# Optimization experiments

Hardware: AMD Instinct MI355X
Metric: run time of the kernel (lower is better)

The kernel has to match this reference:

```python
import jax, jax.numpy as jnp
import numpy as np

N_NODES = 25000
IN_DIM = 16
EDGE_DIM = 8
HID = 32
OUT_DIM = 16
N_EDGES = 400000
MLP_HID = 32


def setup_inputs() -> dict:
    key = jax.random.key(0)
    ks = jax.random.split(key, 12)
    x = jax.random.normal(ks[0], (N_NODES, IN_DIM), dtype=jnp.float32)
    edge_index = jax.random.randint(ks[1], (2, N_EDGES), 0, N_NODES, dtype=jnp.int32)
    edge_attr = jax.random.normal(ks[2], (N_EDGES, EDGE_DIM), dtype=jnp.float32)
    s = lambda fan_in: 1.0 / np.sqrt(fan_in)
    W1 = jax.random.uniform(ks[3], (EDGE_DIM, MLP_HID), minval=-s(EDGE_DIM), maxval=s(EDGE_DIM))
    b1 = jax.random.uniform(ks[4], (MLP_HID,), minval=-s(EDGE_DIM), maxval=s(EDGE_DIM))
    W2 = jax.random.uniform(ks[5], (MLP_HID, IN_DIM * HID), minval=-s(MLP_HID), maxval=s(MLP_HID))
    b2 = jax.random.uniform(ks[6], (IN_DIM * HID,), minval=-s(MLP_HID), maxval=s(MLP_HID))
    root = jax.random.uniform(ks[7], (IN_DIM, HID), minval=-s(IN_DIM), maxval=s(IN_DIM))
    bias = jnp.zeros((HID,), dtype=jnp.float32)
    Wlin = jax.random.uniform(ks[8], (HID, OUT_DIM), minval=-s(HID), maxval=s(HID))
    blin = jax.random.uniform(ks[9], (OUT_DIM,), minval=-s(HID), maxval=s(HID))
    return {"x": x, "edge_attr": edge_attr, "W1": W1, "b1": b1, "W2": W2,
            "b2": b2, "root": root, "bias": bias, "Wlin": Wlin, "blin": blin,
            "edge_index": edge_index}


def reference(x, edge_attr, W1, b1, W2, b2, root, bias, Wlin, blin, edge_index):
    src, dst = edge_index[0], edge_index[1]  # x_j gathered from src, aggregated at dst
    # edge MLP -> per-edge weight matrix [E, IN_DIM, HID]
    h = jax.nn.relu(edge_attr @ W1 + b1)
    W_e = (h @ W2 + b2).reshape(-1, IN_DIM, HID)
    # gather source features and per-edge matvec: [E, HID]
    msg = jnp.einsum('ei,eio->eo', x[src], W_e)
    # scatter-mean over target nodes
    agg = jax.ops.segment_sum(msg, dst, num_segments=N_NODES)
    cnt = jax.ops.segment_sum(jnp.ones((msg.shape[0],), dtype=msg.dtype), dst, num_segments=N_NODES)
    agg = agg / jnp.maximum(cnt, 1.0)[:, None]
    # NNConv root weight + bias, then ReLU and final linear
    out = jax.nn.relu(agg + x @ root + bias)
    return out @ Wlin + blin
```

## Files before the change

kernel.cpp:

```cpp
#include <hip/hip_runtime.h>
#include <cstdint>

#define E_EDGES 400000
#define N_NODES 25000
#define GROUPS  (E_EDGES/16)
#define NPACK   18432

typedef float f32x4 __attribute__((ext_vector_type(4)));
typedef __bf16 bf16x8 __attribute__((ext_vector_type(8)));

static __device__ __forceinline__ ushort f2bf(float f) {
    union { __bf16 b; ushort u; } c; c.b = (__bf16)f; return c.u;
}

__global__ void __launch_bounds__(256) k_pack(const float* __restrict__ W2,
                                              const float* __restrict__ b2,
                                              const float* __restrict__ W1,
                                              ushort* __restrict__ packed) {
    int t = blockIdx.x * 256 + threadIdx.x;
    if (t >= NPACK) return;
    float v = 0.0f;
    if (t < 17408) {
        int j  = t & 7;
        int ln = (t >> 3) & 15;
        int kg = (t >> 7) & 3;
        int nt = (t >> 9) & 1;
        int kt = t >> 10;
        int kap = (j < 4) ? (kg * 4 + j) : (16 + kg * 4 + (j - 4));
        if (kt < 16)       v = W2[kap * 512 + kt * 32 + nt * 16 + ln];
        else if (kap < 16) v = b2[kap * 32 + nt * 16 + ln];
    } else {
        int idx  = t - 17408;
        int half = idx >> 9;
        int lane = (idx >> 3) & 63;
        int j    = idx & 7;
        int kg = lane >> 4, ln = lane & 15;
        if (kg == 0) v = W1[j * 32 + half * 16 + ln];
    }
    packed[t] = f2bf(v);
}

__global__ void __launch_bounds__(256, 4) k_edge(const float* __restrict__ ea,
                                                 const float* __restrict__ x,
                                                 const int* __restrict__ ei,
                                                 const ushort* __restrict__ packed,
                                                 const float* __restrict__ b1,
                                                 float* __restrict__ agg,
                                                 uint* __restrict__ cnt_u) {
    __shared__ alignas(16) ushort w2l[NPACK];
    __shared__ float b1l[32];
    {
        const uint4* s = (const uint4*)packed;
        uint4* d = (uint4*)w2l;
        for (int i = threadIdx.x; i < NPACK / 8; i += 256) d[i] = s[i];
        if (threadIdx.x < 32) b1l[threadIdx.x] = b1[threadIdx.x];
    }
    __syncthreads();

    const int lane = threadIdx.x & 63;
    const int ln = lane & 15;
    const int kg = lane >> 4;
    const int gp = blockIdx.x * 4 + (threadIdx.x >> 6);
    const int g0 = gp * 2, g1 = g0 + 1;
    const int e0 = g0 * 16 + ln, e1 = g1 * 16 + ln;

    const int s0  = ei[e0],            s1  = ei[e1];
    const int dc0 = ei[E_EDGES + e0],  dc1 = ei[E_EDGES + e1];
    const int r0 = g0 * 16 + kg * 4, r1 = g1 * 16 + kg * 4;
    const int d00 = ei[E_EDGES + r0 + 0], d01 = ei[E_EDGES + r0 + 1];
    const int d02 = ei[E_EDGES + r0 + 2], d03 = ei[E_EDGES + r0 + 3];
    const int d10 = ei[E_EDGES + r1 + 0], d11 = ei[E_EDGES + r1 + 1];
    const int d12 = ei[E_EDGES + r1 + 2], d13 = ei[E_EDGES + r1 + 3];

    const f32x4* xp0 = (const f32x4*)(x + (size_t)s0 * 16);
    const f32x4 xa0 = xp0[0], xa1 = xp0[1], xa2 = xp0[2], xa3 = xp0[3];
    const f32x4* xp1 = (const f32x4*)(x + (size_t)s1 * 16);
    const f32x4 xb0 = xp1[0], xb1 = xp1[1], xb2 = xp1[2], xb3 = xp1[3];

    const f32x4* ep0 = (const f32x4*)(ea + (size_t)e0 * 8);
    const f32x4 ea00 = ep0[0], ea01 = ep0[1];
    const f32x4* ep1 = (const f32x4*)(ea + (size_t)e1 * 8);
    const f32x4 ea10 = ep1[0], ea11 = ep1[1];

    bf16x8 eb0, eb1;
    if (kg == 0) {
        eb0[0]=(__bf16)ea00[0]; eb0[1]=(__bf16)ea00[1]; eb0[2]=(__bf16)ea00[2]; eb0[3]=(__bf16)ea00[3];
        eb0[4]=(__bf16)ea01[0]; eb0[5]=(__bf16)ea01[1]; eb0[6]=(__bf16)ea01[2]; eb0[7]=(__bf16)ea01[3];
        eb1[0]=(__bf16)ea10[0]; eb1[1]=(__bf16)ea10[1]; eb1[2]=(__bf16)ea10[2]; eb1[3]=(__bf16)ea10[3];
        eb1[4]=(__bf16)ea11[0]; eb1[5]=(__bf16)ea11[1]; eb1[6]=(__bf16)ea11[2]; eb1[7]=(__bf16)ea11[3];
    } else {
        const __bf16 z = (__bf16)0.0f;
        eb0[0]=z; eb0[1]=z; eb0[2]=z; eb0[3]=z; eb0[4]=z; eb0[5]=z; eb0[6]=z; eb0[7]=z;
        eb1 = eb0;
    }

    const bf16x8 aw0 = *(const bf16x8*)(&w2l[17408 + lane * 8]);
    const bf16x8 aw1 = *(const bf16x8*)(&w2l[17408 + 512 + lane * 8]);
    f32x4 z4 = {0.f, 0.f, 0.f, 0.f};
    f32x4 hA0 = __builtin_amdgcn_mfma_f32_16x16x32_bf16(aw0, eb0, z4, 0, 0, 0);
    f32x4 hA1 = __builtin_amdgcn_mfma_f32_16x16x32_bf16(aw1, eb0, z4, 0, 0, 0);
    f32x4 hB0 = __builtin_amdgcn_mfma_f32_16x16x32_bf16(aw0, eb1, z4, 0, 0, 0);
    f32x4 hB1 = __builtin_amdgcn_mfma_f32_16x16x32_bf16(aw1, eb1, z4, 0, 0, 0);

    float h0[8], h1[8];
#pragma unroll
    for (int r = 0; r < 4; ++r) {
        const float blo = b1l[4 * kg + r], bhi = b1l[16 + 4 * kg + r];
        h0[r]     = fmaxf(hA0[r] + blo, 0.f);
        h0[4 + r] = fmaxf(hA1[r] + bhi, 0.f);
        h1[r]     = fmaxf(hB0[r] + blo, 0.f);
        h1[4 + r] = fmaxf(hB1[r] + bhi, 0.f);
    }

    float xr0[16], xr1[16];
    xr0[0]=xa0[0]; xr0[1]=xa0[1]; xr0[2]=xa0[2]; xr0[3]=xa0[3];
    xr0[4]=xa1[0]; xr0[5]=xa1[1]; xr0[6]=xa1[2]; xr0[7]=xa1[3];
    xr0[8]=xa2[0]; xr0[9]=xa2[1]; xr0[10]=xa2[2]; xr0[11]=xa2[3];
    xr0[12]=xa3[0]; xr0[13]=xa3[1]; xr0[14]=xa3[2]; xr0[15]=xa3[3];
    xr1[0]=xb0[0]; xr1[1]=xb0[1]; xr1[2]=xb0[2]; xr1[3]=xb0[3];
    xr1[4]=xb1[0]; xr1[5]=xb1[1]; xr1[6]=xb1[2]; xr1[7]=xb1[3];
    xr1[8]=xb2[0]; xr1[9]=xb2[1]; xr1[10]=xb2[2]; xr1[11]=xb2[3];
    xr1[12]=xb3[0]; xr1[13]=xb3[1]; xr1[14]=xb3[2]; xr1[15]=xb3[3];

    f32x4 acc00 = z4, acc01 = z4, acc10 = z4, acc11 = z4;

#pragma unroll
    for (int kt = 0; kt < 16; ++kt) {
        const bf16x8 bf0 = *(const bf16x8*)(&w2l[(kt * 2 + 0) * 512 + lane * 8]);
        const bf16x8 bf1 = *(const bf16x8*)(&w2l[(kt * 2 + 1) * 512 + lane * 8]);
        const float xv0 = xr0[kt], xv1 = xr1[kt];
        bf16x8 a0, a1;
#pragma unroll
        for (int j = 0; j < 8; ++j) {
            a0[j] = (__bf16)(xv0 * h0[j]);
            a1[j] = (__bf16)(xv1 * h1[j]);
        }
        acc00 = __builtin_amdgcn_mfma_f32_16x16x32_bf16(a0, bf0, acc00, 0, 0, 0);
        acc10 = __builtin_amdgcn_mfma_f32_16x16x32_bf16(a1, bf0, acc10, 0, 0, 0);
        acc01 = __builtin_amdgcn_mfma_f32_16x16x32_bf16(a0, bf1, acc01, 0, 0, 0);
        acc11 = __builtin_amdgcn_mfma_f32_16x16x32_bf16(a1, bf1, acc11, 0, 0, 0);
    }
    {
        const f32x4 xs0 = (kg == 0) ? xa0 : ((kg == 1) ? xa1 : ((kg == 2) ? xa2 : xa3));
        const f32x4 xs1 = (kg == 0) ? xb0 : ((kg == 1) ? xb1 : ((kg == 2) ? xb2 : xb3));
        const __bf16 z = (__bf16)0.0f;
        bf16x8 a0, a1;
        a0[0]=(__bf16)xs0[0]; a0[1]=(__bf16)xs0[1]; a0[2]=(__bf16)xs0[2]; a0[3]=(__bf16)xs0[3];
        a0[4]=z; a0[5]=z; a0[6]=z; a0[7]=z;
        a1[0]=(__bf16)xs1[0]; a1[1]=(__bf16)xs1[1]; a1[2]=(__bf16)xs1[2]; a1[3]=(__bf16)xs1[3];
        a1[4]=z; a1[5]=z; a1[6]=z; a1[7]=z;
        const bf16x8 bf0 = *(const bf16x8*)(&w2l[(16 * 2 + 0) * 512 + lane * 8]);
        const bf16x8 bf1 = *(const bf16x8*)(&w2l[(16 * 2 + 1) * 512 + lane * 8]);
        acc00 = __builtin_amdgcn_mfma_f32_16x16x32_bf16(a0, bf0, acc00, 0, 0, 0);
        acc10 = __builtin_amdgcn_mfma_f32_16x16x32_bf16(a1, bf0, acc10, 0, 0, 0);
        acc01 = __builtin_amdgcn_mfma_f32_16x16x32_bf16(a0, bf1, acc01, 0, 0, 0);
        acc11 = __builtin_amdgcn_mfma_f32_16x16x32_bf16(a1, bf1, acc11, 0, 0, 0);
    }

    atomicAdd(&agg[d00 * 32 + ln], acc00[0]);
    atomicAdd(&agg[d01 * 32 + ln], acc00[1]);
    atomicAdd(&agg[d02 * 32 + ln], acc00[2]);
    atomicAdd(&agg[d03 * 32 + ln], acc00[3]);
    atomicAdd(&agg[d00 * 32 + 16 + ln], acc01[0]);
    atomicAdd(&agg[d01 * 32 + 16 + ln], acc01[1]);
    atomicAdd(&agg[d02 * 32 + 16 + ln], acc01[2]);
    atomicAdd(&agg[d03 * 32 + 16 + ln], acc01[3]);
    atomicAdd(&agg[d10 * 32 + ln], acc10[0]);
    atomicAdd(&agg[d11 * 32 + ln], acc10[1]);
    atomicAdd(&agg[d12 * 32 + ln], acc10[2]);
    atomicAdd(&agg[d13 * 32 + ln], acc10[3]);
    atomicAdd(&agg[d10 * 32 + 16 + ln], acc11[0]);
    atomicAdd(&agg[d11 * 32 + 16 + ln], acc11[1]);
    atomicAdd(&agg[d12 * 32 + 16 + ln], acc11[2]);
    atomicAdd(&agg[d13 * 32 + 16 + ln], acc11[3]);

    if (kg == 0) {
        atomicAdd(&cnt_u[dc0], 1u);
        atomicAdd(&cnt_u[dc1], 1u);
    }
}

__global__ void __launch_bounds__(256) k_node(const float* __restrict__ agg,
                                              const uint* __restrict__ cnt_u,
                                              const float* __restrict__ x,
                                              const float* __restrict__ root,
                                              const float* __restrict__ bias,
                                              const float* __restrict__ Wlin,
                                              const float* __restrict__ blin,
                                              float* __restrict__ out) {
    __shared__ float al[256];
    const int n0 = blockIdx.x * 8;
    const int t = threadIdx.x;
    const int n = n0 + (t >> 5), h = t & 31;
    float a = 0.0f;
    if (n < N_NODES) {
        const float c = (float)cnt_u[n];
        float s = agg[n * 32 + h] / fmaxf(c, 1.0f) + bias[h];
        const f32x4* xp = (const f32x4*)(x + (size_t)n * 16);
        const f32x4 x0 = xp[0], x1 = xp[1], x2 = xp[2], x3 = xp[3];
        float xv[16];
        xv[0]=x0[0]; xv[1]=x0[1]; xv[2]=x0[2]; xv[3]=x0[3];
        xv[4]=x1[0]; xv[5]=x1[1]; xv[6]=x1[2]; xv[7]=x1[3];
        xv[8]=x2[0]; xv[9]=x2[1]; xv[10]=x2[2]; xv[11]=x2[3];
        xv[12]=x3[0]; xv[13]=x3[1]; xv[14]=x3[2]; xv[15]=x3[3];
#pragma unroll
        for (int i = 0; i < 16; ++i) s += xv[i] * root[i * 32 + h];
        a = fmaxf(s, 0.0f);
    }
    al[t] = a;
    __syncthreads();
    if (t < 128) {
        const int nj = n0 + (t >> 4), j = t & 15;
        if (nj < N_NODES) {
            float s = blin[j];
#pragma unroll
            for (int h2 = 0; h2 < 32; ++h2) s += al[(t >> 4) * 32 + h2] * Wlin[h2 * 16 + j];
            out[nj * 16 + j] = s;
        }
    }
}

extern "C" void kernel_launch(void* const* d_in, const int* in_sizes, int n_in,
                              void* d_out, int out_size, void* d_ws, size_t ws_size,
                              hipStream_t stream) {
    const float* x    = (const float*)d_in[0];
    const float* ea   = (const float*)d_in[1];
    const float* W1   = (const float*)d_in[2];
    const float* b1   = (const float*)d_in[3];
    const float* W2   = (const float*)d_in[4];
    const float* b2   = (const float*)d_in[5];
    const float* root = (const float*)d_in[6];
    const float* bias = (const float*)d_in[7];
    const float* Wlin = (const float*)d_in[8];
    const float* blin = (const float*)d_in[9];
    const int*   ei   = (const int*)d_in[10];
    float* out = (float*)d_out;

    char* ws = (char*)d_ws;
    float*  agg    = (float*)(ws + 0);
    uint*   cnt_u  = (uint*)(ws + 3200000);
    ushort* packed = (ushort*)(ws + 3300000);

    hipMemsetAsync(d_ws, 0, 3300000, stream);

    k_pack<<<(NPACK + 255) / 256, 256, 0, stream>>>(W2, b2, W1, packed);
    k_edge<<<3125, 256, 0, stream>>>(ea, x, ei, packed, b1, agg, cnt_u);
    k_node<<<3125, 256, 0, stream>>>(agg, cnt_u, x, root, bias, Wlin, blin, out);
}
```

Measured before the change: 86.08 us.

## Halve edge-kernel grid with two-unit persistent loop, prefetch, and move counts to pack kernel

The edge kernel now launches about half as many blocks. Each wave processes up to two 32-edge units and prefetches the next unit's indices and edge attributes while computing the current one. This amortizes the per-block LDS weight load, which is about 36 KB. Destination indices are loaded as int4 vectors, and in-degree counting moves into the pack kernel, which now covers all edges. The risks are higher register pressure from the prefetch, the dropped occupancy launch bound, and less parallelism in the edge kernel.

```diff
diff --git a/kernel.cpp b/kernel.cpp
--- a/kernel.cpp
+++ b/kernel.cpp
@@ -3,8 +3,10 @@
 
 #define E_EDGES 400000
 #define N_NODES 25000
-#define GROUPS  (E_EDGES/16)
+#define NU      12500
 #define NPACK   18432
+#define BLOCKS  1563
+#define NWAVES  (BLOCKS*4)
 
 typedef float f32x4 __attribute__((ext_vector_type(4)));
 typedef __bf16 bf16x8 __attribute__((ext_vector_type(8)));
@@ -16,37 +18,40 @@
 __global__ void __launch_bounds__(256) k_pack(const float* __restrict__ W2,
                                               const float* __restrict__ b2,
                                               const float* __restrict__ W1,
-                                              ushort* __restrict__ packed) {
+                                              const int* __restrict__ ei,
+                                              ushort* __restrict__ packed,
+                                              uint* __restrict__ cnt_u) {
     int t = blockIdx.x * 256 + threadIdx.x;
-    if (t >= NPACK) return;
-    float v = 0.0f;
-    if (t < 17408) {
-        int j  = t & 7;
-        int ln = (t >> 3) & 15;
-        int kg = (t >> 7) & 3;
-        int nt = (t >> 9) & 1;
-        int kt = t >> 10;
-        int kap = (j < 4) ? (kg * 4 + j) : (16 + kg * 4 + (j - 4));
-        if (kt < 16)       v = W2[kap * 512 + kt * 32 + nt * 16 + ln];
-        else if (kap < 16) v = b2[kap * 32 + nt * 16 + ln];
-    } else {
-        int idx  = t - 17408;
-        int half = idx >> 9;
-        int lane = (idx >> 3) & 63;
-        int j    = idx & 7;
-        int kg = lane >> 4, ln = lane & 15;
-        if (kg == 0) v = W1[j * 32 + half * 16 + ln];
-    }
-    packed[t] = f2bf(v);
-}
-
-__global__ void __launch_bounds__(256, 4) k_edge(const float* __restrict__ ea,
-                                                 const float* __restrict__ x,
-                                                 const int* __restrict__ ei,
-                                                 const ushort* __restrict__ packed,
-                                                 const float* __restrict__ b1,
-                                                 float* __restrict__ agg,
-                                                 uint* __restrict__ cnt_u) {
+    if (t < NPACK) {
+        float v = 0.0f;
+        if (t < 17408) {
+            int j  = t & 7;
+            int ln = (t >> 3) & 15;
+            int kg = (t >> 7) & 3;
+            int nt = (t >> 9) & 1;
+            int kt = t >> 10;
+            int kap = (j < 4) ? (kg * 4 + j) : (16 + kg * 4 + (j - 4));
+            if (kt < 16)       v = W2[kap * 512 + kt * 32 + nt * 16 + ln];
+            else if (kap < 16) v = b2[kap * 32 + nt * 16 + ln];
+        } else {
+            int idx  = t - 17408;
+            int half = idx >> 9;
+            int lane = (idx >> 3) & 63;
+            int j    = idx & 7;
+            int kg = lane >> 4, ln = lane & 15;
+            if (kg == 0) v = W1[j * 32 + half * 16 + ln];
+        }
+        packed[t] = f2bf(v);
+    }
+    if (t < E_EDGES) atomicAdd(&cnt_u[ei[E_EDGES + t]], 1u);
+}
+
+__global__ void __launch_bounds__(256) k_edge(const float* __restrict__ ea,
+                                              const float* __restrict__ x,
+                                              const int* __restrict__ ei,
+                                              const ushort* __restrict__ packed,
+                                              const float* __restrict__ b1,
+                                              float* __restrict__ agg) {
     __shared__ alignas(16) ushort w2l[NPACK];
     __shared__ float b1l[32];
     {
@@ -60,123 +65,137 @@
     const int lane = threadIdx.x & 63;
     const int ln = lane & 15;
     const int kg = lane >> 4;
-    const int gp = blockIdx.x * 4 + (threadIdx.x >> 6);
-    const int g0 = gp * 2, g1 = g0 + 1;
-    const int e0 = g0 * 16 + ln, e1 = g1 * 16 + ln;
-
-    const int s0  = ei[e0],            s1  = ei[e1];
-    const int dc0 = ei[E_EDGES + e0],  dc1 = ei[E_EDGES + e1];
-    const int r0 = g0 * 16 + kg * 4, r1 = g1 * 16 + kg * 4;
-    const int d00 = ei[E_EDGES + r0 + 0], d01 = ei[E_EDGES + r0 + 1];
-    const int d02 = ei[E_EDGES + r0 + 2], d03 = ei[E_EDGES + r0 + 3];
-    const int d10 = ei[E_EDGES + r1 + 0], d11 = ei[E_EDGES + r1 + 1];
-    const int d12 = ei[E_EDGES + r1 + 2], d13 = ei[E_EDGES + r1 + 3];
-
-    const f32x4* xp0 = (const f32x4*)(x + (size_t)s0 * 16);
-    const f32x4 xa0 = xp0[0], xa1 = xp0[1], xa2 = xp0[2], xa3 = xp0[3];
-    const f32x4* xp1 = (const f32x4*)(x + (size_t)s1 * 16);
-    const f32x4 xb0 = xp1[0], xb1 = xp1[1], xb2 = xp1[2], xb3 = xp1[3];
-
-    const f32x4* ep0 = (const f32x4*)(ea + (size_t)e0 * 8);
-    const f32x4 ea00 = ep0[0], ea01 = ep0[1];
-    const f32x4* ep1 = (const f32x4*)(ea + (size_t)e1 * 8);
-    const f32x4 ea10 = ep1[0], ea11 = ep1[1];
-
-    bf16x8 eb0, eb1;
-    if (kg == 0) {
-        eb0[0]=(__bf16)ea00[0]; eb0[1]=(__bf16)ea00[1]; eb0[2]=(__bf16)ea00[2]; eb0[3]=(__bf16)ea00[3];
-        eb0[4]=(__bf16)ea01[0]; eb0[5]=(__bf16)ea01[1]; eb0[6]=(__bf16)ea01[2]; eb0[7]=(__bf16)ea01[3];
-        eb1[0]=(__bf16)ea10[0]; eb1[1]=(__bf16)ea10[1]; eb1[2]=(__bf16)ea10[2]; eb1[3]=(__bf16)ea10[3];
-        eb1[4]=(__bf16)ea11[0]; eb1[5]=(__bf16)ea11[1]; eb1[6]=(__bf16)ea11[2]; eb1[7]=(__bf16)ea11[3];
-    } else {
-        const __bf16 z = (__bf16)0.0f;
-        eb0[0]=z; eb0[1]=z; eb0[2]=z; eb0[3]=z; eb0[4]=z; eb0[5]=z; eb0[6]=z; eb0[7]=z;
-        eb1 = eb0;
-    }
+    const int wid = blockIdx.x * 4 + (threadIdx.x >> 6);
 
     const bf16x8 aw0 = *(const bf16x8*)(&w2l[17408 + lane * 8]);
     const bf16x8 aw1 = *(const bf16x8*)(&w2l[17408 + 512 + lane * 8]);
-    f32x4 z4 = {0.f, 0.f, 0.f, 0.f};
-    f32x4 hA0 = __builtin_amdgcn_mfma_f32_16x16x32_bf16(aw0, eb0, z4, 0, 0, 0);
-    f32x4 hA1 = __builtin_amdgcn_mfma_f32_16x16x32_bf16(aw1, eb0, z4, 0, 0, 0);
-    f32x4 hB0 = __builtin_amdgcn_mfma_f32_16x16x32_bf16(aw0, eb1, z4, 0, 0, 0);
-    f32x4 hB1 = __builtin_amdgcn_mfma_f32_16x16x32_bf16(aw1, eb1, z4, 0, 0, 0);
-
-    float h0[8], h1[8];
-#pragma unroll
-    for (int r = 0; r < 4; ++r) {
-        const float blo = b1l[4 * kg + r], bhi = b1l[16 + 4 * kg + r];
-        h0[r]     = fmaxf(hA0[r] + blo, 0.f);
-        h0[4 + r] = fmaxf(hA1[r] + bhi, 0.f);
-        h1[r]     = fmaxf(hB0[r] + blo, 0.f);
-        h1[4 + r] = fmaxf(hB1[r] + bhi, 0.f);
-    }
-
-    float xr0[16], xr1[16];
-    xr0[0]=xa0[0]; xr0[1]=xa0[1]; xr0[2]=xa0[2]; xr0[3]=xa0[3];
-    xr0[4]=xa1[0]; xr0[5]=xa1[1]; xr0[6]=xa1[2]; xr0[7]=xa1[3];
-    xr0[8]=xa2[0]; xr0[9]=xa2[1]; xr0[10]=xa2[2]; xr0[11]=xa2[3];
-    xr0[12]=xa3[0]; xr0[13]=xa3[1]; xr0[14]=xa3[2]; xr0[15]=xa3[3];
-    xr1[0]=xb0[0]; xr1[1]=xb0[1]; xr1[2]=xb0[2]; xr1[3]=xb0[3];
-    xr1[4]=xb1[0]; xr1[5]=xb1[1]; xr1[6]=xb1[2]; xr1[7]=xb1[3];
-    xr1[8]=xb2[0]; xr1[9]=xb2[1]; xr1[10]=xb2[2]; xr1[11]=xb2[3];
-    xr1[12]=xb3[0]; xr1[13]=xb3[1]; xr1[14]=xb3[2]; xr1[15]=xb3[3];
-
-    f32x4 acc00 = z4, acc01 = z4, acc10 = z4, acc11 = z4;
-
-#pragma unroll
-    for (int kt = 0; kt < 16; ++kt) {
-        const bf16x8 bf0 = *(const bf16x8*)(&w2l[(kt * 2 + 0) * 512 + lane * 8]);
-        const bf16x8 bf1 = *(const bf16x8*)(&w2l[(kt * 2 + 1) * 512 + lane * 8]);
-        const float xv0 = xr0[kt], xv1 = xr1[kt];
-        bf16x8 a0, a1;
-#pragma unroll
-        for (int j = 0; j < 8; ++j) {
-            a0[j] = (__bf16)(xv0 * h0[j]);
-            a1[j] = (__bf16)(xv1 * h1[j]);
-        }
-        acc00 = __builtin_amdgcn_mfma_f32_16x16x32_bf16(a0, bf0, acc00, 0, 0, 0);
-        acc10 = __builtin_amdgcn_mfma_f32_16x16x32_bf16(a1, bf0, acc10, 0, 0, 0);
-        acc01 = __builtin_amdgcn_mfma_f32_16x16x32_bf16(a0, bf1, acc01, 0, 0, 0);
-        acc11 = __builtin_amdgcn_mfma_f32_16x16x32_bf16(a1, bf1, acc11, 0, 0, 0);
-    }
-    {
-        const f32x4 xs0 = (kg == 0) ? xa0 : ((kg == 1) ? xa1 : ((kg == 2) ? xa2 : xa3));
-        const f32x4 xs1 = (kg == 0) ? xb0 : ((kg == 1) ? xb1 : ((kg == 2) ? xb2 : xb3));
-        const __bf16 z = (__bf16)0.0f;
-        bf16x8 a0, a1;
-        a0[0]=(__bf16)xs0[0]; a0[1]=(__bf16)xs0[1]; a0[2]=(__bf16)xs0[2]; a0[3]=(__bf16)xs0[3];
-        a0[4]=z; a0[5]=z; a0[6]=z; a0[7]=z;
-        a1[0]=(__bf16)xs1[0]; a1[1]=(__bf16)xs1[1]; a1[2]=(__bf16)xs1[2]; a1[3]=(__bf16)xs1[3];
-        a1[4]=z; a1[5]=z; a1[6]=z; a1[7]=z;
-        const bf16x8 bf0 = *(const bf16x8*)(&w2l[(16 * 2 + 0) * 512 + lane * 8]);
-        const bf16x8 bf1 = *(const bf16x8*)(&w2l[(16 * 2 + 1) * 512 + lane * 8]);
-        acc00 = __builtin_amdgcn_mfma_f32_16x16x32_bf16(a0, bf0, acc00, 0, 0, 0);
-        acc10 = __builtin_amdgcn_mfma_f32_16x16x32_bf16(a1, bf0, acc10, 0, 0, 0);
-        acc01 = __builtin_amdgcn_mfma_f32_16x16x32_bf16(a0, bf1, acc01, 0, 0, 0);
-        acc11 = __builtin_amdgcn_mfma_f32_16x16x32_bf16(a1, bf1, acc11, 0, 0, 0);
-    }
-
-    atomicAdd(&agg[d00 * 32 + ln], acc00[0]);
-    atomicAdd(&agg[d01 * 32 + ln], acc00[1]);
-    atomicAdd(&agg[d02 * 32 + ln], acc00[2]);
-    atomicAdd(&agg[d03 * 32 + ln], acc00[3]);
-    atomicAdd(&agg[d00 * 32 + 16 + ln], acc01[0]);
-    atomicAdd(&agg[d01 * 32 + 16 + ln], acc01[1]);
-    atomicAdd(&agg[d02 * 32 + 16 + ln], acc01[2]);
-    atomicAdd(&agg[d03 * 32 + 16 + ln], acc01[3]);
-    atomicAdd(&agg[d10 * 32 + ln], acc10[0]);
-    atomicAdd(&agg[d11 * 32 + ln], acc10[1]);
-    atomicAdd(&agg[d12 * 32 + ln], acc10[2]);
-    atomicAdd(&agg[d13 * 32 + ln], acc10[3]);
-    atomicAdd(&agg[d10 * 32 + 16 + ln], acc11[0]);
-    atomicAdd(&agg[d11 * 32 + 16 + ln], acc11[1]);
-    atomicAdd(&agg[d12 * 32 + 16 + ln], acc11[2]);
-    atomicAdd(&agg[d13 * 32 + 16 + ln], acc11[3]);
-
-    if (kg == 0) {
-        atomicAdd(&cnt_u[dc0], 1u);
-        atomicAdd(&cnt_u[dc1], 1u);
+    const f32x4 z4 = {0.f, 0.f, 0.f, 0.f};
+    const __bf16 zb = (__bf16)0.0f;
+
+    int u = wid;
+    int s0 = ei[u * 32 + ln];
+    int s1 = ei[u * 32 + 16 + ln];
+    int4 d0 = *(const int4*)(ei + E_EDGES + u * 32 + kg * 4);
+    int4 d1 = *(const int4*)(ei + E_EDGES + u * 32 + 16 + kg * 4);
+    const f32x4* ep0 = (const f32x4*)(ea + (size_t)(u * 32 + ln) * 8);
+    f32x4 ea00 = ep0[0], ea01 = ep0[1];
+    const f32x4* ep1 = (const f32x4*)(ea + (size_t)(u * 32 + 16 + ln) * 8);
+    f32x4 ea10 = ep1[0], ea11 = ep1[1];
+
+#pragma unroll
+    for (int it = 0; it < 2; ++it) {
+        const int un = u + NWAVES;
+        const bool pf = (it == 0) && (un < NU);
+
+        const f32x4* xp0 = (const f32x4*)(x + (size_t)s0 * 16);
+        const f32x4 xa0 = xp0[0], xa1 = xp0[1], xa2 = xp0[2], xa3 = xp0[3];
+        const f32x4* xp1 = (const f32x4*)(x + (size_t)s1 * 16);
+        const f32x4 xb0 = xp1[0], xb1 = xp1[1], xb2 = xp1[2], xb3 = xp1[3];
+
+        int ns0 = 0, ns1 = 0;
+        int4 nd0 = {0,0,0,0}, nd1 = {0,0,0,0};
+        f32x4 nea00 = z4, nea01 = z4, nea10 = z4, nea11 = z4;
+        if (pf) {
+            ns0 = ei[un * 32 + ln];
+            ns1 = ei[un * 32 + 16 + ln];
+            nd0 = *(const int4*)(ei + E_EDGES + un * 32 + kg * 4);
+            nd1 = *(const int4*)(ei + E_EDGES + un * 32 + 16 + kg * 4);
+            const f32x4* np0 = (const f32x4*)(ea + (size_t)(un * 32 + ln) * 8);
+            nea00 = np0[0]; nea01 = np0[1];
+            const f32x4* np1 = (const f32x4*)(ea + (size_t)(un * 32 + 16 + ln) * 8);
+            nea10 = np1[0]; nea11 = np1[1];
+        }
+
+        bf16x8 eb0, eb1;
+        if (kg == 0) {
+            eb0[0]=(__bf16)ea00[0]; eb0[1]=(__bf16)ea00[1]; eb0[2]=(__bf16)ea00[2]; eb0[3]=(__bf16)ea00[3];
+            eb0[4]=(__bf16)ea01[0]; eb0[5]=(__bf16)ea01[1]; eb0[6]=(__bf16)ea01[2]; eb0[7]=(__bf16)ea01[3];
+            eb1[0]=(__bf16)ea10[0]; eb1[1]=(__bf16)ea10[1]; eb1[2]=(__bf16)ea10[2]; eb1[3]=(__bf16)ea10[3];
+            eb1[4]=(__bf16)ea11[0]; eb1[5]=(__bf16)ea11[1]; eb1[6]=(__bf16)ea11[2]; eb1[7]=(__bf16)ea11[3];
+        } else {
+            eb0[0]=zb; eb0[1]=zb; eb0[2]=zb; eb0[3]=zb; eb0[4]=zb; eb0[5]=zb; eb0[6]=zb; eb0[7]=zb;
+            eb1 = eb0;
+        }
+        f32x4 hA0 = __builtin_amdgcn_mfma_f32_16x16x32_bf16(aw0, eb0, z4, 0, 0, 0);
+        f32x4 hA1 = __builtin_amdgcn_mfma_f32_16x16x32_bf16(aw1, eb0, z4, 0, 0, 0);
+        f32x4 hB0 = __builtin_amdgcn_mfma_f32_16x16x32_bf16(aw0, eb1, z4, 0, 0, 0);
+        f32x4 hB1 = __builtin_amdgcn_mfma_f32_16x16x32_bf16(aw1, eb1, z4, 0, 0, 0);
+
+        float h0[8], h1[8];
+#pragma unroll
+        for (int r = 0; r < 4; ++r) {
+            const float blo = b1l[4 * kg + r], bhi = b1l[16 + 4 * kg + r];
+            h0[r]     = fmaxf(hA0[r] + blo, 0.f);
+            h0[4 + r] = fmaxf(hA1[r] + bhi, 0.f);
+            h1[r]     = fmaxf(hB0[r] + blo, 0.f);
+            h1[4 + r] = fmaxf(hB1[r] + bhi, 0.f);
+        }
+
+        float xr0[16], xr1[16];
+        xr0[0]=xa0[0]; xr0[1]=xa0[1]; xr0[2]=xa0[2]; xr0[3]=xa0[3];
+        xr0[4]=xa1[0]; xr0[5]=xa1[1]; xr0[6]=xa1[2]; xr0[7]=xa1[3];
+        xr0[8]=xa2[0]; xr0[9]=xa2[1]; xr0[10]=xa2[2]; xr0[11]=xa2[3];
+        xr0[12]=xa3[0]; xr0[13]=xa3[1]; xr0[14]=xa3[2]; xr0[15]=xa3[3];
+        xr1[0]=xb0[0]; xr1[1]=xb0[1]; xr1[2]=xb0[2]; xr1[3]=xb0[3];
+        xr1[4]=xb1[0]; xr1[5]=xb1[1]; xr1[6]=xb1[2]; xr1[7]=xb1[3];
+        xr1[8]=xb2[0]; xr1[9]=xb2[1]; xr1[10]=xb2[2]; xr1[11]=xb2[3];
+        xr1[12]=xb3[0]; xr1[13]=xb3[1]; xr1[14]=xb3[2]; xr1[15]=xb3[3];
+
+        f32x4 acc00 = z4, acc01 = z4, acc10 = z4, acc11 = z4;
+
+#pragma unroll
+        for (int kt = 0; kt < 16; ++kt) {
+            const bf16x8 bf0 = *(const bf16x8*)(&w2l[(kt * 2 + 0) * 512 + lane * 8]);
+            const bf16x8 bf1 = *(const bf16x8*)(&w2l[(kt * 2 + 1) * 512 + lane * 8]);
+            const float xv0 = xr0[kt], xv1 = xr1[kt];
+            bf16x8 a0, a1;
+#pragma unroll
+            for (int j = 0; j < 8; ++j) {
+                a0[j] = (__bf16)(xv0 * h0[j]);
+                a1[j] = (__bf16)(xv1 * h1[j]);
+            }
+            acc00 = __builtin_amdgcn_mfma_f32_16x16x32_bf16(a0, bf0, acc00, 0, 0, 0);
+            acc10 = __builtin_amdgcn_mfma_f32_16x16x32_bf16(a1, bf0, acc10, 0, 0, 0);
+            acc01 = __builtin_amdgcn_mfma_f32_16x16x32_bf16(a0, bf1, acc01, 0, 0, 0);
+            acc11 = __builtin_amdgcn_mfma_f32_16x16x32_bf16(a1, bf1, acc11, 0, 0, 0);
+        }
+        {
+            const f32x4 xs0 = (kg == 0) ? xa0 : ((kg == 1) ? xa1 : ((kg == 2) ? xa2 : xa3));
+            const f32x4 xs1 = (kg == 0) ? xb0 : ((kg == 1) ? xb1 : ((kg == 2) ? xb2 : xb3));
+            bf16x8 a0, a1;
+            a0[0]=(__bf16)xs0[0]; a0[1]=(__bf16)xs0[1]; a0[2]=(__bf16)xs0[2]; a0[3]=(__bf16)xs0[3];
+            a0[4]=zb; a0[5]=zb; a0[6]=zb; a0[7]=zb;
+            a1[0]=(__bf16)xs1[0]; a1[1]=(__bf16)xs1[1]; a1[2]=(__bf16)xs1[2]; a1[3]=(__bf16)xs1[3];
+            a1[4]=zb; a1[5]=zb; a1[6]=zb; a1[7]=zb;
+            const bf16x8 bf0 = *(const bf16x8*)(&w2l[(16 * 2 + 0) * 512 + lane * 8]);
+            const bf16x8 bf1 = *(const bf16x8*)(&w2l[(16 * 2 + 1) * 512 + lane * 8]);
+            acc00 = __builtin_amdgcn_mfma_f32_16x16x32_bf16(a0, bf0, acc00, 0, 0, 0);
+            acc10 = __builtin_amdgcn_mfma_f32_16x16x32_bf16(a1, bf0, acc10, 0, 0, 0);
+            acc01 = __builtin_amdgcn_mfma_f32_16x16x32_bf16(a0, bf1, acc01, 0, 0, 0);
+            acc11 = __builtin_amdgcn_mfma_f32_16x16x32_bf16(a1, bf1, acc11, 0, 0, 0);
+        }
+
+        atomicAdd(&agg[d0.x * 32 + ln],      acc00[0]);
+        atomicAdd(&agg[d0.y * 32 + ln],      acc00[1]);
+        atomicAdd(&agg[d0.z * 32 + ln],      acc00[2]);
+        atomicAdd(&agg[d0.w * 32 + ln],      acc00[3]);
+        atomicAdd(&agg[d0.x * 32 + 16 + ln], acc01[0]);
+        atomicAdd(&agg[d0.y * 32 + 16 + ln], acc01[1]);
+        atomicAdd(&agg[d0.z * 32 + 16 + ln], acc01[2]);
+        atomicAdd(&agg[d0.w * 32 + 16 + ln], acc01[3]);
+        atomicAdd(&agg[d1.x * 32 + ln],      acc10[0]);
+        atomicAdd(&agg[d1.y * 32 + ln],      acc10[1]);
+        atomicAdd(&agg[d1.z * 32 + ln],      acc10[2]);
+        atomicAdd(&agg[d1.w * 32 + ln],      acc10[3]);
+        atomicAdd(&agg[d1.x * 32 + 16 + ln], acc11[0]);
+        atomicAdd(&agg[d1.y * 32 + 16 + ln], acc11[1]);
+        atomicAdd(&agg[d1.z * 32 + 16 + ln], acc11[2]);
+        atomicAdd(&agg[d1.w * 32 + 16 + ln], acc11[3]);
+
+        if (!pf) break;
+        u = un;
+        s0 = ns0; s1 = ns1; d0 = nd0; d1 = nd1;
+        ea00 = nea00; ea01 = nea01; ea10 = nea10; ea11 = nea11;
     }
 }
 
@@ -243,7 +262,7 @@
 
     hipMemsetAsync(d_ws, 0, 3300000, stream);
 
-    k_pack<<<(NPACK + 255) / 256, 256, 0, stream>>>(W2, b2, W1, packed);
-    k_edge<<<3125, 256, 0, stream>>>(ea, x, ei, packed, b1, agg, cnt_u);
+    k_pack<<<BLOCKS, 256, 0, stream>>>(W2, b2, W1, ei, packed, cnt_u);
+    k_edge<<<BLOCKS, 256, 0, stream>>>(ea, x, ei, packed, b1, agg);
     k_node<<<3125, 256, 0, stream>>>(agg, cnt_u, x, root, bias, Wlin, blin, out);
 }
```

Result: slower. 90.29 us (+4.9%).
